# Performance work log

Hardware: AMD Instinct MI355X
Metric: run time of the kernel (lower is better)

Reference implementation:

```python
import jax, jax.numpy as jnp
import numpy as np

B, T, C, H = 128, 256, 384, 6
HS = C // H  # 64
EPS = 1e-5


def _ln(x, g, b):
    mu = jnp.mean(x, axis=-1, keepdims=True)
    var = jnp.mean(jnp.square(x - mu), axis=-1, keepdims=True)
    return (x - mu) * jax.lax.rsqrt(var + EPS) * g + b


def setup_inputs() -> dict:
    key = jax.random.key(0)
    ks = jax.random.split(key, 12)
    s = 0.02
    return {
        "x": jax.random.normal(ks[0], (B, T, C), jnp.float32),
        "wq": jax.random.normal(ks[1], (H, C, HS), jnp.float32) * s,
        "wk": jax.random.normal(ks[2], (H, C, HS), jnp.float32) * s,
        "wv": jax.random.normal(ks[3], (H, C, HS), jnp.float32) * s,
        "w_proj": jax.random.normal(ks[4], (C, C), jnp.float32) * s,
        "b_proj": jax.random.normal(ks[5], (C,), jnp.float32) * s,
        "w1": jax.random.normal(ks[6], (C, 4 * C), jnp.float32) * s,
        "b1": jax.random.normal(ks[7], (4 * C,), jnp.float32) * s,
        "w2": jax.random.normal(ks[8], (4 * C, C), jnp.float32) * s,
        "b2": jax.random.normal(ks[9], (C,), jnp.float32) * s,
        "ln1_g": 1.0 + jax.random.normal(ks[10], (C,), jnp.float32) * s,
        "ln1_b": jnp.zeros((C,), jnp.float32),
        "ln2_g": 1.0 + jax.random.normal(ks[11], (C,), jnp.float32) * s,
        "ln2_b": jnp.zeros((C,), jnp.float32),
    }


def reference(x, wq, wk, wv, w_proj, b_proj, w1, b1, w2, b2, ln1_g, ln1_b, ln2_g, ln2_b):
    # --- attention sublayer (dropout = identity, eval mode) ---
    h = _ln(x, ln1_g, ln1_b)                              # (B,T,C)
    q = jnp.einsum("btc,hcd->bhtd", h, wq)               # (B,H,T,HS)
    k = jnp.einsum("btc,hcd->bhtd", h, wk)
    v = jnp.einsum("btc,hcd->bhtd", h, wv)
    # NOTE: original scales by n_embed**-0.5 (C), not head_size**-0.5
    wei = jnp.einsum("bhtd,bhsd->bhts", q, k) * (C ** -0.5)  # (B,H,T,T)
    tril = jnp.tril(jnp.ones((T, T), bool))
    wei = jnp.where(tril, wei, -jnp.inf)
    # NOTE: original applies softmax over torch dim=1 of (B,T,T) = query axis
    wei = jax.nn.softmax(wei, axis=2)
    attn = jnp.einsum("bhts,bhsd->bhtd", wei, v)          # (B,H,T,HS)
    attn = attn.transpose(0, 2, 1, 3).reshape(B, T, C)    # head-concat order
    x = x + attn @ w_proj + b_proj
    # --- MLP sublayer ---
    h2 = _ln(x, ln2_g, ln2_b)
    x = x + jax.nn.relu(h2 @ w1 + b1) @ w2 + b2
    return x
```

## Files before the change

kernel.cpp:

```cpp
#include <hip/hip_runtime.h>

#define BB 128
#define TT 256
#define CCH 384
#define NHH 6
#define HSZ 64
#define BTT (BB*TT)
#define QKVLD 1152

typedef unsigned short u16;
typedef unsigned int   u32;
typedef __attribute__((ext_vector_type(8))) short  short8;
typedef __attribute__((ext_vector_type(4))) float  floatx4;

__device__ __forceinline__ u16 f2bf(float f) {
  union { float f; u32 i; } v; v.f = f; u32 x = v.i;
  return (u16)((x + 0x7fffu + ((x >> 16) & 1u)) >> 16);
}
__device__ __forceinline__ float bf2f(u16 w) {
  union { u32 i; float f; } v; v.i = ((u32)w) << 16; return v.f;
}

__device__ __forceinline__ void gll16(const u16* g, u16* l) {
  __builtin_amdgcn_global_load_lds((const __attribute__((address_space(1))) void*)g,
                                   (__attribute__((address_space(3))) void*)l, 16, 0, 0);
}

template <int INBF>
__global__ __launch_bounds__(256) void ln_kernel(const void* __restrict__ xv,
                                                 const float* __restrict__ g,
                                                 const float* __restrict__ b,
                                                 u16* __restrict__ out) {
  int row = blockIdx.x * 4 + (threadIdx.x >> 6);
  int lane = threadIdx.x & 63;
  float vals[6];
  float sum = 0.f;
  if (INBF) {
    const u16* xr = (const u16*)xv + (size_t)row * CCH;
#pragma unroll
    for (int i = 0; i < 6; ++i) { vals[i] = bf2f(xr[lane + (i << 6)]); sum += vals[i]; }
  } else {
    const float* xr = (const float*)xv + (size_t)row * CCH;
#pragma unroll
    for (int i = 0; i < 6; ++i) { vals[i] = xr[lane + (i << 6)]; sum += vals[i]; }
  }
#pragma unroll
  for (int off = 32; off; off >>= 1) sum += __shfl_xor(sum, off);
  float mean = sum * (1.f / 384.f);
  float vs = 0.f;
#pragma unroll
  for (int i = 0; i < 6; ++i) { float d = vals[i] - mean; vs += d * d; }
#pragma unroll
  for (int off = 32; off; off >>= 1) vs += __shfl_xor(vs, off);
  float rinv = rsqrtf(vs * (1.f / 384.f) + 1e-5f);
  u16* orow = out + (size_t)row * CCH;
#pragma unroll
  for (int i = 0; i < 6; ++i) {
    int c = lane + (i << 6);
    orow[c] = f2bf((vals[i] - mean) * rinv * g[c] + b[c]);
  }
}

__global__ void repack_all(const float* __restrict__ wq, const float* __restrict__ wk,
                           const float* __restrict__ wv, const float* __restrict__ wproj,
                           const float* __restrict__ w1, const float* __restrict__ w2,
                           u16* __restrict__ wqkv_t, u16* __restrict__ wp_t,
                           u16* __restrict__ w1_t, u16* __restrict__ w2_t) {
  int idx = blockIdx.x * 256 + threadIdx.x;
  const int S1 = 442368;
  const int S2 = S1 + 147456;
  const int S3 = S2 + 589824;
  const int S4 = S3 + 589824;
  if (idx < S1) {
    int i = idx, e = i & 7, l = (i >> 3) & 63, r = i >> 9;
    int kt = r % 12, nb = r / 12;
    int n = nb * 16 + (l & 15), k = kt * 32 + (l >> 4) * 8 + e;
    int sel = n / 384, nn = n % 384;
    size_t src = ((size_t)(nn >> 6) * 384 + k) * 64 + (nn & 63);
    float v = (sel == 0) ? wq[src] : (sel == 1) ? wk[src] : wv[src];
    wqkv_t[i] = f2bf(v);
  } else if (idx < S2) {
    int i = idx - S1, e = i & 7, l = (i >> 3) & 63, r = i >> 9;
    int kt = r % 12, nb = r / 12;
    int n = nb * 16 + (l & 15), k = kt * 32 + (l >> 4) * 8 + e;
    wp_t[i] = f2bf(wproj[(size_t)k * 384 + n]);
  } else if (idx < S3) {
    int i = idx - S2, e = i & 7, l = (i >> 3) & 63, r = i >> 9;
    int kt = r % 12, nb = r / 12;
    int n = nb * 16 + (l & 15), k = kt * 32 + (l >> 4) * 8 + e;
    w1_t[i] = f2bf(w1[(size_t)k * 1536 + n]);
  } else if (idx < S4) {
    int i = idx - S3, e = i & 7, l = (i >> 3) & 63, r = i >> 9;
    int kt = r % 48, nb = r / 48;
    int n = nb * 16 + (l & 15), k = kt * 32 + (l >> 4) * 8 + e;
    w2_t[i] = f2bf(w2[(size_t)k * 384 + n]);
  }
}

template <int BIAS, int RES, int RELU, int OUTBF, int RESBF>
__global__ __launch_bounds__(192, 2) void gemm_kres3(const u16* __restrict__ A,
                                                     const u16* __restrict__ Bp,
                                                     const float* __restrict__ bias,
                                                     const void* __restrict__ resv,
                                                     void* __restrict__ outv,
                                                     int M, int N) {
  __shared__ __align__(16) u16 Ah[12 * 2048];
  const int tid = threadIdx.x;
  const int lane = tid & 63;
  const int w = tid >> 6;

  const int gx = gridDim.x;
  const int nwg = gx * gridDim.y;
  const int bid = blockIdx.y * gx + blockIdx.x;
  const int lin = (bid & 7) * (nwg >> 3) + (bid >> 3);
  const int m0 = (lin / gx) * 64, n0 = (lin % gx) * 192;

  const int lm = lane & 15, qd = lane >> 4;

#pragma unroll
  for (int g = 0; g < 16; ++g) {
    int call = w * 16 + g;
    int kt = call >> 2, c = call & 3;
    int row = 16 * c + (lane >> 2);
    int ch = (lane & 3) ^ ((row >> 1) & 3);
    const u16* src = A + (size_t)(m0 + row) * 384 + kt * 32 + ch * 8;
    gll16(src, &Ah[kt * 2048 + c * 512]);
  }

  const u16* bsrc[4];
#pragma unroll
  for (int j = 0; j < 4; ++j)
    bsrc[j] = Bp + ((size_t)((n0 >> 4) + 4 * w + j) * 12) * 512 + lane * 8;

  floatx4 acc[4][4];
  floatx4 zero4 = {0.f, 0.f, 0.f, 0.f};
#pragma unroll
  for (int i = 0; i < 4; ++i)
#pragma unroll
    for (int j = 0; j < 4; ++j) acc[i][j] = zero4;

  short8 bA[4], bB[4];
#pragma unroll
  for (int j = 0; j < 4; ++j) bA[j] = *(const short8*)(bsrc[j]);

  asm volatile("s_waitcnt vmcnt(0)" ::: "memory");
  __syncthreads();

#pragma unroll
  for (int k2 = 0; k2 < 6; ++k2) {
    {
      const int kt = 2 * k2;
#pragma unroll
      for (int j = 0; j < 4; ++j) bB[j] = *(const short8*)(bsrc[j] + (kt + 1) * 512);
      short8 af[4];
#pragma unroll
      for (int i = 0; i < 4; ++i) {
        int rm = 16 * i + lm;
        af[i] = *(const short8*)&Ah[kt * 2048 + rm * 32 + (qd ^ ((rm >> 1) & 3)) * 8];
      }
#pragma unroll
      for (int i = 0; i < 4; ++i)
#pragma unroll
        for (int j = 0; j < 4; ++j)
          acc[i][j] = __builtin_amdgcn_mfma_f32_16x16x32_bf16(af[i], bA[j], acc[i][j], 0, 0, 0);
    }
    {
      const int kt = 2 * k2 + 1;
      if (kt < 11) {
#pragma unroll
        for (int j = 0; j < 4; ++j) bA[j] = *(const short8*)(bsrc[j] + (kt + 1) * 512);
      }
      short8 af[4];
#pragma unroll
      for (int i = 0; i < 4; ++i) {
        int rm = 16 * i + lm;
        af[i] = *(const short8*)&Ah[kt * 2048 + rm * 32 + (qd ^ ((rm >> 1) & 3)) * 8];
      }
#pragma unroll
      for (int i = 0; i < 4; ++i)
#pragma unroll
        for (int j = 0; j < 4; ++j)
          acc[i][j] = __builtin_amdgcn_mfma_f32_16x16x32_bf16(af[i], bB[j], acc[i][j], 0, 0, 0);
    }
  }

#pragma unroll
  for (int i = 0; i < 4; ++i) {
    int row0 = m0 + 16 * i + qd * 4;
#pragma unroll
    for (int j = 0; j < 4; ++j) {
      int col = n0 + 64 * w + 16 * j + lm;
      float bb = 0.f;
      if (BIAS) bb = bias[col];
#pragma unroll
      for (int r = 0; r < 4; ++r) {
        size_t idx = (size_t)(row0 + r) * N + col;
        float val = acc[i][j][r] + bb;
        if (RES) val += RESBF ? bf2f(((const u16*)resv)[idx]) : ((const float*)resv)[idx];
        if (RELU) val = fmaxf(val, 0.f);
        if (OUTBF) ((u16*)outv)[idx] = f2bf(val);
        else       ((float*)outv)[idx] = val;
      }
    }
  }
}

template <int BIAS, int RES, int RELU, int OUTBF, int RESBF>
__global__ __launch_bounds__(256, 3) void gemm_mfma(const u16* __restrict__ A,
                                                    const u16* __restrict__ Bp,
                                                    const float* __restrict__ bias,
                                                    const void* __restrict__ resv,
                                                    void* __restrict__ outv,
                                                    int M, int N, int K) {
  __shared__ __align__(16) u16 As[2][128 * 32];
  const int tid = threadIdx.x;
  const int lane = tid & 63;
  const int w = tid >> 6;
  const int wr = w >> 1, wc = w & 1;

  const int gx = gridDim.x;
  const int nwg = gx * gridDim.y;
  const int bid = blockIdx.y * gx + blockIdx.x;
  const int lin = (bid & 7) * (nwg >> 3) + (bid >> 3);
  const int m0 = (lin / gx) * 128, n0 = (lin % gx) * 128;

  const int lm = lane & 15, qd = lane >> 4;
  const int KT = K >> 5;

  floatx4 acc[4][4];
  floatx4 zero4 = {0.f, 0.f, 0.f, 0.f};
#pragma unroll
  for (int i = 0; i < 4; ++i)
#pragma unroll
    for (int j = 0; j < 4; ++j) acc[i][j] = zero4;

  const u16* srcA[2];
#pragma unroll
  for (int c = 0; c < 2; ++c) {
    int row = 32 * w + 16 * c + (lane >> 2);
    int ch = (lane & 3) ^ ((row >> 1) & 3);
    srcA[c] = A + (size_t)(m0 + row) * K + ch * 8;
  }
  const int dA = (32 * w) * 32;

  const u16* bsrc[4];
#pragma unroll
  for (int j = 0; j < 4; ++j)
    bsrc[j] = Bp + ((size_t)((n0 >> 4) + 4 * wc + j) * KT) * 512 + lane * 8;

#pragma unroll
  for (int c = 0; c < 2; ++c) gll16(srcA[c], &As[0][dA + 512 * c]);
  short8 bcur[4], bnxt[4];
#pragma unroll
  for (int j = 0; j < 4; ++j) bcur[j] = *(const short8*)(bsrc[j]);

  for (int k0 = 0; k0 < K; k0 += 64) {
    __syncthreads();
    {
      int kn = k0 + 32;
      int kto = (kn >> 5) << 9;
#pragma unroll
      for (int j = 0; j < 4; ++j) bnxt[j] = *(const short8*)(bsrc[j] + kto);
#pragma unroll
      for (int c = 0; c < 2; ++c) gll16(srcA[c] + kn, &As[1][dA + 512 * c]);
      short8 af[4];
#pragma unroll
      for (int i = 0; i < 4; ++i) {
        int rm = 64 * wr + 16 * i + lm;
        af[i] = *(const short8*)&As[0][rm * 32 + (qd ^ ((rm >> 1) & 3)) * 8];
      }
#pragma unroll
      for (int i = 0; i < 4; ++i)
#pragma unroll
        for (int j = 0; j < 4; ++j)
          acc[i][j] = __builtin_amdgcn_mfma_f32_16x16x32_bf16(af[i], bcur[j], acc[i][j], 0, 0, 0);
    }
    __syncthreads();
    {
      int kn = k0 + 64;
      if (kn < K) {
        int kto = (kn >> 5) << 9;
#pragma unroll
        for (int j = 0; j < 4; ++j) bcur[j] = *(const short8*)(bsrc[j] + kto);
#pragma unroll
        for (int c = 0; c < 2; ++c) gll16(srcA[c] + kn, &As[0][dA + 512 * c]);
      }
      short8 af[4];
#pragma unroll
      for (int i = 0; i < 4; ++i) {
        int rm = 64 * wr + 16 * i + lm;
        af[i] = *(const short8*)&As[1][rm * 32 + (qd ^ ((rm >> 1) & 3)) * 8];
      }
#pragma unroll
      for (int i = 0; i < 4; ++i)
#pragma unroll
        for (int j = 0; j < 4; ++j)
          acc[i][j] = __builtin_amdgcn_mfma_f32_16x16x32_bf16(af[i], bnxt[j], acc[i][j], 0, 0, 0);
    }
  }

#pragma unroll
  for (int i = 0; i < 4; ++i) {
    int row0 = m0 + 64 * wr + 16 * i + qd * 4;
#pragma unroll
    for (int j = 0; j < 4; ++j) {
      int col = n0 + 64 * wc + 16 * j + lm;
      float bb = 0.f;
      if (BIAS) bb = bias[col];
#pragma unroll
      for (int r = 0; r < 4; ++r) {
        size_t idx = (size_t)(row0 + r) * N + col;
        float val = acc[i][j][r] + bb;
        if (RES) val += RESBF ? bf2f(((const u16*)resv)[idx]) : ((const float*)resv)[idx];
        if (RELU) val = fmaxf(val, 0.f);
        if (OUTBF) ((u16*)outv)[idx] = f2bf(val);
        else       ((float*)outv)[idx] = val;
      }
    }
  }
}

#define ASCALE 0.051031036307982884f

__global__ __launch_bounds__(1024) void attn_mfma(const u16* __restrict__ qkv,
                                                  u16* __restrict__ out) {
  __shared__ __align__(16) char lds_raw[36864 + 20480 + 2048];
  u16*   Ks       = (u16*)lds_raw;
  u16*   VT       = (u16*)lds_raw;
  float* partials = (float*)(lds_raw + 36864);
  u16*   stage    = (u16*)(lds_raw + 36864);
  float* gmax     = (float*)(lds_raw + 57344);
  float* linv     = (float*)(lds_raw + 58368);

  const int tid = threadIdx.x;
  const int lane = tid & 63;
  const int w = tid >> 6;
  const int lm = lane & 15, qd = lane >> 4;
  const int b = blockIdx.x / NHH, h = blockIdx.x % NHH;
  const size_t rowbase = (size_t)b * TT;
  const u16* qp = qkv + rowbase * QKVLD + h * HSZ;
  const u16* kp = qp + 384;
  const u16* vp = qp + 768;

  {
    int s = tid >> 2, c4 = tid & 3;
    const u16* src = kp + (size_t)s * QKVLD;
    *(uint4*)&Ks[s * 72 + c4 * 8]       = *(const uint4*)(src + c4 * 8);
    *(uint4*)&Ks[s * 72 + (c4 + 4) * 8] = *(const uint4*)(src + (c4 + 4) * 8);
  }
  short8 qf0, qf1;
  {
    const u16* qrow = qp + (size_t)(16 * w + lm) * QKVLD + qd * 8;
    qf0 = *(const short8*)(qrow);
    qf1 = *(const short8*)(qrow + 32);
  }
  __syncthreads();

  floatx4 acc[16];
  floatx4 zero4 = {0.f, 0.f, 0.f, 0.f};
#pragma unroll
  for (int tc = 0; tc < 16; ++tc) acc[tc] = zero4;

#pragma unroll
  for (int tc = 0; tc < 16; ++tc) {
    if (tc <= w) {
      int sr = 16 * tc + lm;
      short8 kf0 = *(const short8*)&Ks[sr * 72 + qd * 8];
      short8 kf1 = *(const short8*)&Ks[sr * 72 + 32 + qd * 8];
      acc[tc] = __builtin_amdgcn_mfma_f32_16x16x32_bf16(qf0, kf0, acc[tc], 0, 0, 0);
      acc[tc] = __builtin_amdgcn_mfma_f32_16x16x32_bf16(qf1, kf1, acc[tc], 0, 0, 0);
    }
  }

  const int rb = 16 * w + qd * 4;
  float pmax[16];
#pragma unroll
  for (int tc = 0; tc < 16; ++tc) {
    float m = -1e30f;
    if (tc <= w) {
      int sc = 16 * tc + lm;
#pragma unroll
      for (int r = 0; r < 4; ++r) {
        float vv = acc[tc][r] * ASCALE;
        vv = (rb + r >= sc) ? vv : -1e30f;
        acc[tc][r] = vv;
        m = fmaxf(m, vv);
      }
    }
    m = fmaxf(m, __shfl_xor(m, 16));
    m = fmaxf(m, __shfl_xor(m, 32));
    pmax[tc] = m;
  }
  if (lane < 16) {
#pragma unroll
    for (int tc = 0; tc < 16; ++tc) partials[w * 256 + tc * 16 + lane] = pmax[tc];
  }
  __syncthreads();
  if (tid < 256) {
    float m = partials[tid];
#pragma unroll
    for (int i = 1; i < 16; ++i) m = fmaxf(m, partials[i * 256 + tid]);
    gmax[tid] = m;
  }
  __syncthreads();

  float psum[16];
#pragma unroll
  for (int tc = 0; tc < 16; ++tc) {
    float s = 0.f;
    if (tc <= w) {
      float gm = gmax[tc * 16 + lm];
#pragma unroll
      for (int r = 0; r < 4; ++r) {
        float e = (acc[tc][r] > -1e29f) ? __expf(acc[tc][r] - gm) : 0.f;
        acc[tc][r] = e;
        s += e;
      }
    }
    s += __shfl_xor(s, 16);
    s += __shfl_xor(s, 32);
    psum[tc] = s;
  }
  if (lane < 16) {
#pragma unroll
    for (int tc = 0; tc < 16; ++tc) partials[w * 256 + tc * 16 + lane] = psum[tc];
  }
  __syncthreads();
  if (tid < 256) {
    float s = partials[tid];
#pragma unroll
    for (int i = 1; i < 16; ++i) s += partials[i * 256 + tid];
    linv[tid] = 1.f / s;
  }
  __syncthreads();

  {
    int s = tid >> 2, dg = (tid & 3) * 16;
    const u16* vrow = vp + (size_t)s * QKVLD + dg;
    u16 tmp[16];
    *(uint4*)&tmp[0] = *(const uint4*)(vrow);
    *(uint4*)&tmp[8] = *(const uint4*)(vrow + 8);
#pragma unroll
    for (int j = 0; j < 16; ++j) VT[(dg + j) * 264 + s] = tmp[j];
  }
  __syncthreads();

  u16* mst = stage + w * 640;
  floatx4 oacc[4];
#pragma unroll
  for (int nt = 0; nt < 4; ++nt) oacc[nt] = zero4;

#pragma unroll
  for (int c = 0; c < 8; ++c) {
    if (2 * c <= w) {
#pragma unroll
      for (int tt = 0; tt < 2; ++tt) {
        int tc = 2 * c + tt;
        float li = (tc <= w) ? linv[tc * 16 + lm] : 0.f;
#pragma unroll
        for (int r = 0; r < 4; ++r) {
          float pv = (tc <= w) ? acc[tc][r] * li : 0.f;
          mst[(qd * 4 + r) * 40 + tt * 16 + lm] = f2bf(pv);
        }
      }
      asm volatile("s_waitcnt lgkmcnt(0)" ::: "memory");
      short8 pf = *(const short8*)&mst[lm * 40 + qd * 8];
#pragma unroll
      for (int nt = 0; nt < 4; ++nt) {
        short8 vf = *(const short8*)&VT[(nt * 16 + lm) * 264 + c * 32 + qd * 8];
        oacc[nt] = __builtin_amdgcn_mfma_f32_16x16x32_bf16(pf, vf, oacc[nt], 0, 0, 0);
      }
      asm volatile("" ::: "memory");
    }
  }

  u16* ob = out + rowbase * CCH + h * HSZ;
#pragma unroll
  for (int nt = 0; nt < 4; ++nt) {
#pragma unroll
    for (int r = 0; r < 4; ++r) {
      int t = 16 * w + qd * 4 + r;
      ob[(size_t)t * CCH + nt * 16 + lm] = f2bf(oacc[nt][r]);
    }
  }
}

extern "C" void kernel_launch(void* const* d_in, const int* in_sizes, int n_in,
                              void* d_out, int out_size, void* d_ws, size_t ws_size,
                              hipStream_t stream) {
  const float* x     = (const float*)d_in[0];
  const float* wq    = (const float*)d_in[1];
  const float* wk    = (const float*)d_in[2];
  const float* wv    = (const float*)d_in[3];
  const float* wproj = (const float*)d_in[4];
  const float* bproj = (const float*)d_in[5];
  const float* w1    = (const float*)d_in[6];
  const float* b1    = (const float*)d_in[7];
  const float* w2    = (const float*)d_in[8];
  const float* b2    = (const float*)d_in[9];
  const float* ln1g  = (const float*)d_in[10];
  const float* ln1b  = (const float*)d_in[11];
  const float* ln2g  = (const float*)d_in[12];
  const float* ln2b  = (const float*)d_in[13];
  float* out = (float*)d_out;
  (void)in_sizes; (void)n_in; (void)out_size; (void)ws_size;

  char* ws = (char*)d_ws;
  size_t off = 0;
  auto alloc = [&](size_t bytes) -> void* {
    void* p = ws + off;
    off += (bytes + 255) & ~(size_t)255;
    return p;
  };

  u16* wqkv_t = (u16*)alloc((size_t)QKVLD * CCH * 2);
  u16* wp_t   = (u16*)alloc((size_t)CCH * CCH * 2);
  u16* w1_t   = (u16*)alloc((size_t)4 * CCH * CCH * 2);
  u16* w2_t   = (u16*)alloc((size_t)CCH * 4 * CCH * 2);
  u16*   h_b  = (u16*)alloc((size_t)BTT * CCH * 2);
  u16*   x2   = (u16*)alloc((size_t)BTT * CCH * 2);
  u16*   qkv_b = (u16*)alloc((size_t)BTT * 4 * CCH * 2);
  u16*   u_b   = qkv_b;

  repack_all<<<6912, 256, 0, stream>>>(wq, wk, wv, wproj, w1, w2,
                                       wqkv_t, wp_t, w1_t, w2_t);

  ln_kernel<0><<<BTT / 4, 256, 0, stream>>>(x, ln1g, ln1b, h_b);

  gemm_kres3<0, 0, 0, 1, 0><<<dim3(6, 512), 192, 0, stream>>>(h_b, wqkv_t, nullptr, nullptr,
                                                              qkv_b, BTT, QKVLD);
  attn_mfma<<<BB * NHH, 1024, 0, stream>>>(qkv_b, h_b);

  gemm_kres3<1, 1, 0, 1, 0><<<dim3(2, 512), 192, 0, stream>>>(h_b, wp_t, bproj, x, x2,
                                                              BTT, CCH);
  ln_kernel<1><<<BTT / 4, 256, 0, stream>>>(x2, ln2g, ln2b, h_b);

  gemm_kres3<1, 0, 1, 1, 0><<<dim3(8, 512), 192, 0, stream>>>(h_b, w1_t, b1, nullptr, u_b,
                                                              BTT, 4 * CCH);
  gemm_mfma<1, 1, 0, 0, 1><<<dim3(3, 256), 256, 0, stream>>>(u_b, w2_t, b2, x2, out,
                                                             BTT, CCH, 4 * CCH);
}
```

Baseline: 338.4 us.

## Fuse attention projection with LayerNorm2 and widen GEMM tiles to 384 columns

New measurement: 383.1 us. 13.2% more time.

```diff
diff --git a/kernel.cpp b/kernel.cpp
--- a/kernel.cpp
+++ b/kernel.cpp
@@ -98,7 +98,7 @@
 }
 
 template <int BIAS, int RES, int RELU, int OUTBF, int RESBF>
-__global__ __launch_bounds__(192, 2) void gemm_kres3(const u16* __restrict__ A,
+__global__ __launch_bounds__(384, 4) void gemm_kres6(const u16* __restrict__ A,
                                                      const u16* __restrict__ Bp,
                                                      const float* __restrict__ bias,
                                                      const void* __restrict__ resv,
@@ -113,13 +113,13 @@
   const int nwg = gx * gridDim.y;
   const int bid = blockIdx.y * gx + blockIdx.x;
   const int lin = (bid & 7) * (nwg >> 3) + (bid >> 3);
-  const int m0 = (lin / gx) * 64, n0 = (lin % gx) * 192;
+  const int m0 = (lin / gx) * 64, n0 = (lin % gx) * 384;
 
   const int lm = lane & 15, qd = lane >> 4;
 
 #pragma unroll
-  for (int g = 0; g < 16; ++g) {
-    int call = w * 16 + g;
+  for (int g = 0; g < 8; ++g) {
+    int call = w * 8 + g;
     int kt = call >> 2, c = call & 3;
     int row = 16 * c + (lane >> 2);
     int ch = (lane & 3) ^ ((row >> 1) & 3);
@@ -200,6 +200,156 @@
         if (RELU) val = fmaxf(val, 0.f);
         if (OUTBF) ((u16*)outv)[idx] = f2bf(val);
         else       ((float*)outv)[idx] = val;
+      }
+    }
+  }
+}
+
+__global__ __launch_bounds__(384, 2) void proj_ln2(const u16* __restrict__ A,
+                                                   const u16* __restrict__ Bp,
+                                                   const float* __restrict__ bias,
+                                                   const float* __restrict__ xres,
+                                                   const float* __restrict__ g2,
+                                                   const float* __restrict__ b2,
+                                                   u16* __restrict__ x2out,
+                                                   u16* __restrict__ hout) {
+  __shared__ __align__(16) u16 Ah[12 * 2048];
+  __shared__ float part[64][8][2];
+  __shared__ float sLN[64][2];
+  const int tid = threadIdx.x;
+  const int lane = tid & 63;
+  const int w = tid >> 6;
+
+  const int nwg = gridDim.x;
+  const int bid = blockIdx.x;
+  const int lin = (bid & 7) * (nwg >> 3) + (bid >> 3);
+  const int m0 = lin * 64;
+
+  const int lm = lane & 15, qd = lane >> 4;
+
+#pragma unroll
+  for (int g = 0; g < 8; ++g) {
+    int call = w * 8 + g;
+    int kt = call >> 2, c = call & 3;
+    int row = 16 * c + (lane >> 2);
+    int ch = (lane & 3) ^ ((row >> 1) & 3);
+    const u16* src = A + (size_t)(m0 + row) * 384 + kt * 32 + ch * 8;
+    gll16(src, &Ah[kt * 2048 + c * 512]);
+  }
+
+  const u16* bsrc[4];
+#pragma unroll
+  for (int j = 0; j < 4; ++j)
+    bsrc[j] = Bp + ((size_t)(4 * w + j) * 12) * 512 + lane * 8;
+
+  floatx4 acc[4][4];
+  floatx4 zero4 = {0.f, 0.f, 0.f, 0.f};
+#pragma unroll
+  for (int i = 0; i < 4; ++i)
+#pragma unroll
+    for (int j = 0; j < 4; ++j) acc[i][j] = zero4;
+
+  short8 bA[4], bB[4];
+#pragma unroll
+  for (int j = 0; j < 4; ++j) bA[j] = *(const short8*)(bsrc[j]);
+
+  asm volatile("s_waitcnt vmcnt(0)" ::: "memory");
+  __syncthreads();
+
+#pragma unroll
+  for (int k2 = 0; k2 < 6; ++k2) {
+    {
+      const int kt = 2 * k2;
+#pragma unroll
+      for (int j = 0; j < 4; ++j) bB[j] = *(const short8*)(bsrc[j] + (kt + 1) * 512);
+      short8 af[4];
+#pragma unroll
+      for (int i = 0; i < 4; ++i) {
+        int rm = 16 * i + lm;
+        af[i] = *(const short8*)&Ah[kt * 2048 + rm * 32 + (qd ^ ((rm >> 1) & 3)) * 8];
+      }
+#pragma unroll
+      for (int i = 0; i < 4; ++i)
+#pragma unroll
+        for (int j = 0; j < 4; ++j)
+          acc[i][j] = __builtin_amdgcn_mfma_f32_16x16x32_bf16(af[i], bA[j], acc[i][j], 0, 0, 0);
+    }
+    {
+      const int kt = 2 * k2 + 1;
+      if (kt < 11) {
+#pragma unroll
+        for (int j = 0; j < 4; ++j) bA[j] = *(const short8*)(bsrc[j] + (kt + 1) * 512);
+      }
+      short8 af[4];
+#pragma unroll
+      for (int i = 0; i < 4; ++i) {
+        int rm = 16 * i + lm;
+        af[i] = *(const short8*)&Ah[kt * 2048 + rm * 32 + (qd ^ ((rm >> 1) & 3)) * 8];
+      }
+#pragma unroll
+      for (int i = 0; i < 4; ++i)
+#pragma unroll
+        for (int j = 0; j < 4; ++j)
+          acc[i][j] = __builtin_amdgcn_mfma_f32_16x16x32_bf16(af[i], bB[j], acc[i][j], 0, 0, 0);
+    }
+  }
+
+#pragma unroll
+  for (int i = 0; i < 4; ++i) {
+#pragma unroll
+    for (int j = 0; j < 4; ++j) {
+      int col = 64 * w + 16 * j + lm;
+      float bb = bias[col];
+#pragma unroll
+      for (int r = 0; r < 4; ++r) {
+        size_t idx = (size_t)(m0 + 16 * i + qd * 4 + r) * 384 + col;
+        float val = acc[i][j][r] + bb + xres[idx];
+        acc[i][j][r] = val;
+        x2out[idx] = f2bf(val);
+      }
+    }
+  }
+#pragma unroll
+  for (int i = 0; i < 4; ++i) {
+#pragma unroll
+    for (int r = 0; r < 4; ++r) {
+      float s = 0.f, q = 0.f;
+#pragma unroll
+      for (int j = 0; j < 4; ++j) { float v = acc[i][j][r]; s += v; q += v * v; }
+#pragma unroll
+      for (int off = 1; off < 16; off <<= 1) {
+        s += __shfl_xor(s, off);
+        q += __shfl_xor(q, off);
+      }
+      if (lm == 0) {
+        int rl = 16 * i + qd * 4 + r;
+        part[rl][w][0] = s;
+        part[rl][w][1] = q;
+      }
+    }
+  }
+  __syncthreads();
+  if (tid < 64) {
+    float S = 0.f, Q = 0.f;
+#pragma unroll
+    for (int ww = 0; ww < 6; ++ww) { S += part[tid][ww][0]; Q += part[tid][ww][1]; }
+    float mean = S * (1.f / 384.f);
+    float var = Q * (1.f / 384.f) - mean * mean;
+    sLN[tid][0] = mean;
+    sLN[tid][1] = rsqrtf(var + 1e-5f);
+  }
+  __syncthreads();
+#pragma unroll
+  for (int i = 0; i < 4; ++i) {
+#pragma unroll
+    for (int j = 0; j < 4; ++j) {
+      int col = 64 * w + 16 * j + lm;
+      float gg = g2[col], b22 = b2[col];
+#pragma unroll
+      for (int r = 0; r < 4; ++r) {
+        int rl = 16 * i + qd * 4 + r;
+        float mean = sLN[rl][0], ri = sLN[rl][1];
+        hout[(size_t)(m0 + rl) * 384 + col] = f2bf((acc[i][j][r] - mean) * ri * gg + b22);
       }
     }
   }
@@ -527,15 +677,13 @@
 
   ln_kernel<0><<<BTT / 4, 256, 0, stream>>>(x, ln1g, ln1b, h_b);
 
-  gemm_kres3<0, 0, 0, 1, 0><<<dim3(6, 512), 192, 0, stream>>>(h_b, wqkv_t, nullptr, nullptr,
+  gemm_kres6<0, 0, 0, 1, 0><<<dim3(3, 512), 384, 0, stream>>>(h_b, wqkv_t, nullptr, nullptr,
                                                               qkv_b, BTT, QKVLD);
   attn_mfma<<<BB * NHH, 1024, 0, stream>>>(qkv_b, h_b);
 
-  gemm_kres3<1, 1, 0, 1, 0><<<dim3(2, 512), 192, 0, stream>>>(h_b, wp_t, bproj, x, x2,
-                                                              BTT, CCH);
-  ln_kernel<1><<<BTT / 4, 256, 0, stream>>>(x2, ln2g, ln2b, h_b);
-
-  gemm_kres3<1, 0, 1, 1, 0><<<dim3(8, 512), 192, 0, stream>>>(h_b, w1_t, b1, nullptr, u_b,
+  proj_ln2<<<512, 384, 0, stream>>>(h_b, wp_t, bproj, x, ln2g, ln2b, x2, h_b);
+
+  gemm_kres6<1, 0, 1, 1, 0><<<dim3(4, 512), 384, 0, stream>>>(h_b, w1_t, b1, nullptr, u_b,
                                                               BTT, 4 * CCH);
   gemm_mfma<1, 1, 0, 0, 1><<<dim3(3, 256), 256, 0, stream>>>(u_b, w2_t, b2, x2, out,
                                                              BTT, CCH, 4 * CCH);
```
